# Kernel optimization log

Measured on AMD Instinct MI355X. Metric: run time of the kernel, lower is better.

Reference implementation:

```python
import jax, jax.numpy as jnp
import numpy as np
from jax import lax

# NARX hyperparameters (match init_kwargs)
D_I, D_O, D_X, D_Y, D_HL = 8, 8, 32, 16, 256
B, T = 2048, 512
IN_SIZE = D_I * D_X + D_O * D_Y  # 384


def setup_inputs() -> dict:
    key = jax.random.key(0)
    k1, k2, k3, k4, k5 = jax.random.split(key, 5)
    s1 = 1.0 / np.sqrt(IN_SIZE).astype(np.float32)
    s2 = 1.0 / np.sqrt(D_HL).astype(np.float32)
    x = jax.random.normal(k1, (B, T, D_X), dtype=jnp.float32)
    W1 = jax.random.uniform(k2, (D_HL, IN_SIZE), jnp.float32, -s1, s1)
    b1 = jax.random.uniform(k3, (D_HL,), jnp.float32, -s1, s1)
    W2 = jax.random.uniform(k4, (D_Y, D_HL), jnp.float32, -s2, s2)
    b2 = jax.random.uniform(k5, (D_Y,), jnp.float32, -s2, s2)
    return {"x": x, "W1": W1, "b1": b1, "W2": W2, "b2": b2}


def reference(x, W1, b1, W2, b2):
    # Closed-loop NARX: mode='close', y=None, bootstrap=None.
    # y_pred starts as zeros; loop runs from max(d_i, d_o) to T.
    Bb, Tt, _ = x.shape
    start = max(D_I, D_O)

    def step(hist, t):
        # hist: [B, d_o, d_y], oldest first == y_pred[:, t-d_o:t, :]
        xw = lax.dynamic_slice_in_dim(x, t - D_I, D_I, axis=1).reshape(Bb, D_I * D_X)
        inp = jnp.concatenate([xw, hist.reshape(Bb, D_O * D_Y)], axis=1)
        h = jnp.tanh(inp @ W1.T + b1)
        out = jax.nn.sigmoid(h @ W2.T + b2)  # act2 = Sigmoid
        new_hist = jnp.concatenate([hist[:, 1:, :], out[:, None, :]], axis=1)
        return new_hist, out

    hist0 = jnp.zeros((Bb, D_O, D_Y), dtype=x.dtype)  # zero-initialized y_pred history
    _, outs = lax.scan(step, hist0, jnp.arange(start, Tt))
    outs = jnp.transpose(outs, (1, 0, 2))  # [B, T-start, d_y]
    prefix = jnp.zeros((Bb, start, D_Y), dtype=x.dtype)
    return jnp.concatenate([prefix, outs], axis=1)  # [B, T, d_y]
```

## Files before the change

kernel.cpp:

```cpp
#include <hip/hip_runtime.h>
#include <hip/hip_bf16.h>


typedef short bf16x8 __attribute__((ext_vector_type(8)));
typedef float f32x4  __attribute__((ext_vector_type(4)));

#define MFMA16(A,B,C) __builtin_amdgcn_mfma_f32_16x16x32_bf16((A),(B),(C),0,0,0)

constexpr int DT = 512;
constexpr int DX = 32;
constexpr int DY = 16;
constexpr int BB = 16;

constexpr int XROW  = 40;
constexpr int XSLOT = 16 * XROW;
constexpr int YROW  = 24;
constexpr int YSLOT = 16 * YROW;
constexpr int HROW  = 264;
constexpr int PROW  = 17;
constexpr int PWAVE = 16 * PROW;

__device__ __forceinline__ short bfbits(float f) {
  return __builtin_bit_cast(short, (__bf16)f);
}
__device__ __forceinline__ float fast_tanh(float a) {
  float e = __expf(2.0f * a);
  return 1.0f - 2.0f * __builtin_amdgcn_rcpf(e + 1.0f);
}
__device__ __forceinline__ float fast_sigmoid(float a) {
  return __builtin_amdgcn_rcpf(1.0f + __expf(-a));
}

__global__ __launch_bounds__(512, 2) void narx_kernel(
    const float* __restrict__ x,  const float* __restrict__ W1,
    const float* __restrict__ b1, const float* __restrict__ W2,
    const float* __restrict__ b2, float* __restrict__ out)
{
  __shared__ __align__(16) short xbuf[8 * XSLOT];
  __shared__ __align__(16) short ybuf[8 * YSLOT];
  __shared__ __align__(16) short hbuf[16 * HROW];
  __shared__ __align__(16) float pbuf[8 * PWAVE];

  const int tid  = threadIdx.x;
  const int lane = tid & 63;
  const int w    = tid >> 6;
  const int lm   = lane & 15;
  const int lg   = lane >> 4;
  const int b0   = blockIdx.x * BB;

  bf16x8 wf[2][12];
#pragma unroll
  for (int ti = 0; ti < 2; ++ti) {
    const int n = w * 32 + ti * 16 + lm;
#pragma unroll
    for (int c = 0; c < 12; ++c) {
      const float* p = W1 + n * 384 + c * 32 + lg * 8;
      bf16x8 v;
#pragma unroll
      for (int j = 0; j < 8; ++j) v[j] = bfbits(p[j]);
      wf[ti][c] = v;
    }
  }
  bf16x8 w2fp;
  {
    const float* p = W2 + lm * 256 + w * 32 + lg * 8;
    bf16x8 v;
#pragma unroll
    for (int j = 0; j < 8; ++j) v[j] = bfbits(p[j]);
    w2fp = v;
  }
  const float b1v0 = b1[w * 32 + lm];
  const float b1v1 = b1[w * 32 + 16 + lm];
  const float b2v  = b2[lm];

  {
    const int m = tid >> 5, off = (tid & 31) * 4;
    f32x4 z = {0.f, 0.f, 0.f, 0.f};
    *reinterpret_cast<f32x4*>(out + (size_t)(b0 + m) * (DT * DY) + off) = z;
  }

  {
    const int m = tid >> 5, k = tid & 31;
#pragma unroll
    for (int tt = 0; tt < 8; ++tt)
      xbuf[tt * XSLOT + m * XROW + k] =
          bfbits(x[(size_t)(b0 + m) * (DT * DX) + tt * DX + k]);
    for (int i = tid; i < 8 * YSLOT; i += 512) ybuf[i] = 0;
  }
  __syncthreads();

  const int pm = tid >> 5, pk = tid & 31;

  for (int t = 8; t < DT; ++t) {
    const float xv = x[(size_t)(b0 + pm) * (DT * DX) + t * DX + pk];

    bf16x8 af[12];
#pragma unroll
    for (int c = 0; c < 8; ++c) {
      const int slot = (t + c) & 7;
      af[c] = *reinterpret_cast<const bf16x8*>(
          &xbuf[slot * XSLOT + lm * XROW + lg * 8]);
    }
#pragma unroll
    for (int c = 0; c < 4; ++c) {
      const int i    = c * 2 + (lg >> 1);
      const int slot = (t + i) & 7;
      af[8 + c] = *reinterpret_cast<const bf16x8*>(
          &ybuf[slot * YSLOT + lm * YROW + (lg & 1) * 8]);
    }
    f32x4 acc0a = {0.f, 0.f, 0.f, 0.f}, acc0b = {0.f, 0.f, 0.f, 0.f};
    f32x4 acc1a = {0.f, 0.f, 0.f, 0.f}, acc1b = {0.f, 0.f, 0.f, 0.f};
#pragma unroll
    for (int c = 0; c < 6; ++c) {
      acc0a = MFMA16(af[c],     wf[0][c],     acc0a);
      acc1a = MFMA16(af[c],     wf[1][c],     acc1a);
      acc0b = MFMA16(af[c + 6], wf[0][c + 6], acc0b);
      acc1b = MFMA16(af[c + 6], wf[1][c + 6], acc1b);
    }
#pragma unroll
    for (int r = 0; r < 4; ++r) {
      const int row = lg * 4 + r;
      const float h0 = fast_tanh(acc0a[r] + acc0b[r] + b1v0);
      const float h1 = fast_tanh(acc1a[r] + acc1b[r] + b1v1);
      hbuf[row * HROW + w * 32 + lm]      = bfbits(h0);
      hbuf[row * HROW + w * 32 + 16 + lm] = bfbits(h1);
    }

    bf16x8 ha = *reinterpret_cast<const bf16x8*>(
        &hbuf[lm * HROW + w * 32 + lg * 8]);
    f32x4 zero = {0.f, 0.f, 0.f, 0.f};
    f32x4 part = MFMA16(ha, w2fp, zero);
#pragma unroll
    for (int r = 0; r < 4; ++r)
      pbuf[w * PWAVE + (lg * 4 + r) * PROW + lm] = part[r];
    __syncthreads();

    if (tid < 256) {
      const int row = tid >> 4, col = tid & 15;
      float s = b2v;
#pragma unroll
      for (int ww = 0; ww < 8; ++ww)
        s += pbuf[ww * PWAVE + row * PROW + col];
      const float o = fast_sigmoid(s);
      ybuf[(t & 7) * YSLOT + row * YROW + col] = bfbits(o);
      out[(size_t)(b0 + row) * (DT * DY) + t * DY + col] = o;
    }
    xbuf[(t & 7) * XSLOT + pm * XROW + pk] = bfbits(xv);
    __syncthreads();
  }
}

extern "C" void kernel_launch(void* const* d_in, const int* in_sizes, int n_in,
                              void* d_out, int out_size, void* d_ws, size_t ws_size,
                              hipStream_t stream) {
  const float* x  = (const float*)d_in[0];
  const float* W1 = (const float*)d_in[1];
  const float* b1 = (const float*)d_in[2];
  const float* W2 = (const float*)d_in[3];
  const float* b2 = (const float*)d_in[4];
  float* out = (float*)d_out;
  narx_kernel<<<dim3(128), dim3(512), 0, stream>>>(x, W1, b1, W2, b2, out);
}
```

Measured before the change: 765.6 us.

## Keep x window in registers, per-wave swizzled h buffer, unroll time loop by 8

```diff
diff --git a/kernel.cpp b/kernel.cpp
--- a/kernel.cpp
+++ b/kernel.cpp
@@ -12,12 +12,11 @@
 constexpr int DY = 16;
 constexpr int BB = 16;
 
-constexpr int XROW  = 40;
-constexpr int XSLOT = 16 * XROW;
 constexpr int YROW  = 24;
 constexpr int YSLOT = 16 * YROW;
-constexpr int HROW  = 264;
-constexpr int PROW  = 17;
+constexpr int HROW  = 40;
+constexpr int HWAVE = 16 * HROW;
+constexpr int PROW  = 18;
 constexpr int PWAVE = 16 * PROW;
 
 __device__ __forceinline__ short bfbits(float f) {
@@ -36,9 +35,8 @@
     const float* __restrict__ b1, const float* __restrict__ W2,
     const float* __restrict__ b2, float* __restrict__ out)
 {
-  __shared__ __align__(16) short xbuf[8 * XSLOT];
   __shared__ __align__(16) short ybuf[8 * YSLOT];
-  __shared__ __align__(16) short hbuf[16 * HROW];
+  __shared__ __align__(16) short hbuf[8 * HWAVE];
   __shared__ __align__(16) float pbuf[8 * PWAVE];
 
   const int tid  = threadIdx.x;
@@ -79,75 +77,100 @@
     *reinterpret_cast<f32x4*>(out + (size_t)(b0 + m) * (DT * DY) + off) = z;
   }
 
-  {
-    const int m = tid >> 5, k = tid & 31;
+  const float* xlane = x + (size_t)(b0 + lm) * (DT * DX) + lg * 8;
+  bf16x8 xr[8];
 #pragma unroll
-    for (int tt = 0; tt < 8; ++tt)
-      xbuf[tt * XSLOT + m * XROW + k] =
-          bfbits(x[(size_t)(b0 + m) * (DT * DX) + tt * DX + k]);
-    for (int i = tid; i < 8 * YSLOT; i += 512) ybuf[i] = 0;
+  for (int s = 0; s < 8; ++s) {
+    f32x4 a = *reinterpret_cast<const f32x4*>(xlane + s * DX);
+    f32x4 b = *reinterpret_cast<const f32x4*>(xlane + s * DX + 4);
+    bf16x8 v;
+#pragma unroll
+    for (int j = 0; j < 4; ++j) { v[j] = bfbits(a[j]); v[4 + j] = bfbits(b[j]); }
+    xr[s] = v;
   }
+  f32x4 gA0 = *reinterpret_cast<const f32x4*>(xlane + 8 * DX);
+  f32x4 gA1 = *reinterpret_cast<const f32x4*>(xlane + 8 * DX + 4);
+  f32x4 gB0 = gA0, gB1 = gA1;
+
+  for (int i = tid; i < 8 * YSLOT; i += 512) ybuf[i] = 0;
   __syncthreads();
 
-  const int pm = tid >> 5, pk = tid & 31;
+  const int yhalf  = lg >> 1;
+  const int yoff   = lm * YROW + (lg & 1) * 8;
+  const int hw_w   = w * HWAVE;
+  const int hswz_w = lg << 3;
+  const int hread  = hw_w + ((lm * HROW + lg * 8) ^ (((lm >> 2) & 3) << 3));
+  const int pw     = w * PWAVE;
+  const int rrow   = tid >> 4, rcol = tid & 15;
 
-  for (int t = 8; t < DT; ++t) {
-    const float xv = x[(size_t)(b0 + pm) * (DT * DX) + t * DX + pk];
+#define STEP(U, CUR0, CUR1, NXT0, NXT1)                                        \
+  do {                                                                         \
+    const int t = tb + (U);                                                    \
+    { const int tl = (t + 1 < DT) ? (t + 1) : (DT - 1);                        \
+      NXT0 = *reinterpret_cast<const f32x4*>(xlane + tl * DX);                 \
+      NXT1 = *reinterpret_cast<const f32x4*>(xlane + tl * DX + 4); }           \
+    bf16x8 ay0, ay1, ay2, ay3;                                                 \
+    ay0 = *reinterpret_cast<const bf16x8*>(                                    \
+        &ybuf[((((U) + 0 + yhalf) & 7) * YSLOT) + yoff]);                      \
+    ay1 = *reinterpret_cast<const bf16x8*>(                                    \
+        &ybuf[((((U) + 2 + yhalf) & 7) * YSLOT) + yoff]);                      \
+    ay2 = *reinterpret_cast<const bf16x8*>(                                    \
+        &ybuf[((((U) + 4 + yhalf) & 7) * YSLOT) + yoff]);                      \
+    ay3 = *reinterpret_cast<const bf16x8*>(                                    \
+        &ybuf[((((U) + 6 + yhalf) & 7) * YSLOT) + yoff]);                      \
+    f32x4 acc0a = {0.f,0.f,0.f,0.f}, acc0b = {0.f,0.f,0.f,0.f};                \
+    f32x4 acc1a = {0.f,0.f,0.f,0.f}, acc1b = {0.f,0.f,0.f,0.f};                \
+    _Pragma("unroll") for (int c = 0; c < 6; ++c) {                            \
+      acc0a = MFMA16(xr[((U) + c) & 7], wf[0][c], acc0a);                      \
+      acc1a = MFMA16(xr[((U) + c) & 7], wf[1][c], acc1a);                      \
+    }                                                                          \
+    acc0b = MFMA16(xr[((U) + 6) & 7], wf[0][6], acc0b);                        \
+    acc1b = MFMA16(xr[((U) + 6) & 7], wf[1][6], acc1b);                        \
+    acc0b = MFMA16(xr[((U) + 7) & 7], wf[0][7], acc0b);                        \
+    acc1b = MFMA16(xr[((U) + 7) & 7], wf[1][7], acc1b);                        \
+    acc0b = MFMA16(ay0, wf[0][8],  acc0b);  acc1b = MFMA16(ay0, wf[1][8],  acc1b); \
+    acc0b = MFMA16(ay1, wf[0][9],  acc0b);  acc1b = MFMA16(ay1, wf[1][9],  acc1b); \
+    acc0b = MFMA16(ay2, wf[0][10], acc0b);  acc1b = MFMA16(ay2, wf[1][10], acc1b); \
+    acc0b = MFMA16(ay3, wf[0][11], acc0b);  acc1b = MFMA16(ay3, wf[1][11], acc1b); \
+    { bf16x8 nx;                                                               \
+      _Pragma("unroll") for (int j = 0; j < 4; ++j) {                          \
+        nx[j] = bfbits(CUR0[j]); nx[4 + j] = bfbits(CUR1[j]); }                \
+      xr[(U) & 7] = nx; }                                                      \
+    _Pragma("unroll") for (int r = 0; r < 4; ++r) {                            \
+      const int row = lg * 4 + r;                                              \
+      const float h0 = fast_tanh(acc0a[r] + acc0b[r] + b1v0);                  \
+      const float h1 = fast_tanh(acc1a[r] + acc1b[r] + b1v1);                  \
+      hbuf[hw_w + ((row * HROW + lm) ^ hswz_w)]      = bfbits(h0);             \
+      hbuf[hw_w + ((row * HROW + 16 + lm) ^ hswz_w)] = bfbits(h1);             \
+    }                                                                          \
+    bf16x8 ha = *reinterpret_cast<const bf16x8*>(&hbuf[hread]);                \
+    f32x4 pz = {0.f, 0.f, 0.f, 0.f};                                           \
+    f32x4 part = MFMA16(ha, w2fp, pz);                                         \
+    _Pragma("unroll") for (int r = 0; r < 4; ++r)                              \
+      pbuf[pw + (lg * 4 + r) * PROW + lm] = part[r];                           \
+    __syncthreads();                                                           \
+    if (tid < 256) {                                                           \
+      float s = b2v;                                                           \
+      _Pragma("unroll") for (int ww = 0; ww < 8; ++ww)                         \
+        s += pbuf[ww * PWAVE + rrow * PROW + rcol];                            \
+      const float o = fast_sigmoid(s);                                         \
+      ybuf[((U) & 7) * YSLOT + rrow * YROW + rcol] = bfbits(o);                \
+      out[(size_t)(b0 + rrow) * (DT * DY) + t * DY + rcol] = o;                \
+    }                                                                          \
+    __syncthreads();                                                           \
+  } while (0)
 
-    bf16x8 af[12];
-#pragma unroll
-    for (int c = 0; c < 8; ++c) {
-      const int slot = (t + c) & 7;
-      af[c] = *reinterpret_cast<const bf16x8*>(
-          &xbuf[slot * XSLOT + lm * XROW + lg * 8]);
-    }
-#pragma unroll
-    for (int c = 0; c < 4; ++c) {
-      const int i    = c * 2 + (lg >> 1);
-      const int slot = (t + i) & 7;
-      af[8 + c] = *reinterpret_cast<const bf16x8*>(
-          &ybuf[slot * YSLOT + lm * YROW + (lg & 1) * 8]);
-    }
-    f32x4 acc0a = {0.f, 0.f, 0.f, 0.f}, acc0b = {0.f, 0.f, 0.f, 0.f};
-    f32x4 acc1a = {0.f, 0.f, 0.f, 0.f}, acc1b = {0.f, 0.f, 0.f, 0.f};
-#pragma unroll
-    for (int c = 0; c < 6; ++c) {
-      acc0a = MFMA16(af[c],     wf[0][c],     acc0a);
-      acc1a = MFMA16(af[c],     wf[1][c],     acc1a);
-      acc0b = MFMA16(af[c + 6], wf[0][c + 6], acc0b);
-      acc1b = MFMA16(af[c + 6], wf[1][c + 6], acc1b);
-    }
-#pragma unroll
-    for (int r = 0; r < 4; ++r) {
-      const int row = lg * 4 + r;
-      const float h0 = fast_tanh(acc0a[r] + acc0b[r] + b1v0);
-      const float h1 = fast_tanh(acc1a[r] + acc1b[r] + b1v1);
-      hbuf[row * HROW + w * 32 + lm]      = bfbits(h0);
-      hbuf[row * HROW + w * 32 + 16 + lm] = bfbits(h1);
-    }
-
-    bf16x8 ha = *reinterpret_cast<const bf16x8*>(
-        &hbuf[lm * HROW + w * 32 + lg * 8]);
-    f32x4 zero = {0.f, 0.f, 0.f, 0.f};
-    f32x4 part = MFMA16(ha, w2fp, zero);
-#pragma unroll
-    for (int r = 0; r < 4; ++r)
-      pbuf[w * PWAVE + (lg * 4 + r) * PROW + lm] = part[r];
-    __syncthreads();
-
-    if (tid < 256) {
-      const int row = tid >> 4, col = tid & 15;
-      float s = b2v;
-#pragma unroll
-      for (int ww = 0; ww < 8; ++ww)
-        s += pbuf[ww * PWAVE + row * PROW + col];
-      const float o = fast_sigmoid(s);
-      ybuf[(t & 7) * YSLOT + row * YROW + col] = bfbits(o);
-      out[(size_t)(b0 + row) * (DT * DY) + t * DY + col] = o;
-    }
-    xbuf[(t & 7) * XSLOT + pm * XROW + pk] = bfbits(xv);
-    __syncthreads();
+  for (int tb = 8; tb < DT; tb += 8) {
+    STEP(0, gA0, gA1, gB0, gB1);
+    STEP(1, gB0, gB1, gA0, gA1);
+    STEP(2, gA0, gA1, gB0, gB1);
+    STEP(3, gB0, gB1, gA0, gA1);
+    STEP(4, gA0, gA1, gB0, gB1);
+    STEP(5, gB0, gB1, gA0, gA1);
+    STEP(6, gA0, gA1, gB0, gB1);
+    STEP(7, gB0, gB1, gA0, gA1);
   }
+#undef STEP
 }
 
 extern "C" void kernel_launch(void* const* d_in, const int* in_sizes, int n_in,
```

New measurement: 649.9 us. -15.1%, faster.
